# Performance work log

Hardware: AMD Instinct MI355X
Metric: run time of the kernel (lower is better)

## Reference

```python
import jax, jax.numpy as jnp
import numpy as np

NUM_EMBEDDINGS = 4096
EMBEDDING_DIM = 64
COMMITMENT_COST = 0.25


def setup_inputs() -> dict:
    key = jax.random.key(0)
    kz, kw = jax.random.split(key)
    z = jax.random.normal(kz, (16, 4096, EMBEDDING_DIM), dtype=jnp.float32)
    # torch init: uniform_(-1/num_embeddings, 1/num_embeddings)
    W = jax.random.uniform(kw, (NUM_EMBEDDINGS, EMBEDDING_DIM), dtype=jnp.float32,
                           minval=-1.0 / NUM_EMBEDDINGS, maxval=1.0 / NUM_EMBEDDINGS)
    return {"z": z, "W": W}


def reference(z, W):
    d = W.shape[1]
    zf = z.reshape(-1, d)  # [N, d]
    # squared L2 distances via expansion: ||z||^2 + ||w||^2 - 2 z.w -> [N, K]
    distances = (jnp.sum(zf * zf, axis=1, keepdims=True)
                 + jnp.sum(W * W, axis=1)
                 - 2.0 * jnp.matmul(zf, W.T))
    idx = jnp.argmin(distances, axis=1)          # [N]
    z_q = W[idx].reshape(z.shape)                # gather codebook vectors
    loss = jnp.mean(jnp.square(z - jax.lax.stop_gradient(z_q))) * COMMITMENT_COST
    z_q_out = z + jax.lax.stop_gradient(z_q - z)  # straight-through estimator
    return loss, z_q_out
```

## Files before the change

### kernel.cpp

```cpp
#include <hip/hip_runtime.h>
#include <stdint.h>

typedef short short8 __attribute__((ext_vector_type(8)));
typedef float floatx4 __attribute__((ext_vector_type(4)));

#define BIAS 8.0f

__device__ __forceinline__ unsigned short f2bf(float f) {
    unsigned int u = __float_as_uint(f);
    unsigned int r = (u + 0x7FFFu + ((u >> 16) & 1u)) >> 16;
    return (unsigned short)r;
}

__global__ void vq_prep(const float* __restrict__ W, unsigned short* __restrict__ Wsw,
                        float* __restrict__ out0) {
    const int s = blockIdx.x * 256 + threadIdx.x;
    const int T = s >> 7;
    const int h = (s >> 6) & 1;
    const int l = s & 63;
    const int code = T * 16 + (l & 15);
    const float* src = W + code * 64 + h * 32 + (l >> 4) * 8;
    const floatx4* sp = (const floatx4*)src;
    floatx4 f0 = sp[0], f1 = sp[1];
    short8 fr;
    fr[0] = (short)f2bf(-f0[0]); fr[1] = (short)f2bf(-f0[1]);
    fr[2] = (short)f2bf(-f0[2]); fr[3] = (short)f2bf(-f0[3]);
    fr[4] = (short)f2bf(-f1[0]); fr[5] = (short)f2bf(-f1[1]);
    fr[6] = (short)f2bf(-f1[2]); fr[7] = (short)f2bf(-f1[3]);
    ((short8*)Wsw)[s] = fr;
    if (s == 0) *out0 = 0.0f;
}

__launch_bounds__(256)
__attribute__((amdgpu_waves_per_eu(4, 4)))
__global__ void vq_main(const float* __restrict__ z, const float* __restrict__ W,
                        const unsigned short* __restrict__ Wsw, float* __restrict__ out) {
    __shared__ unsigned int pk_lds[256];
    __shared__ float ls[4];

    const int tid  = threadIdx.x;
    const int lane = tid & 63;
    const int cg   = tid >> 6;
    const int l15  = lane & 15;
    const int lq   = lane >> 4;
    const int rowbase = blockIdx.x * 64;

    short8 afrag[4][2];
    #pragma unroll
    for (int mt = 0; mt < 4; ++mt) {
        const float* zp = z + (rowbase + mt * 16 + l15) * 64 + lq * 8;
        #pragma unroll
        for (int h = 0; h < 2; ++h) {
            const floatx4* p = (const floatx4*)(zp + h * 32);
            floatx4 f0 = p[0], f1 = p[1];
            short8 fr;
            fr[0] = (short)f2bf(f0[0]); fr[1] = (short)f2bf(f0[1]);
            fr[2] = (short)f2bf(f0[2]); fr[3] = (short)f2bf(f0[3]);
            fr[4] = (short)f2bf(f1[0]); fr[5] = (short)f2bf(f1[1]);
            fr[6] = (short)f2bf(f1[2]); fr[7] = (short)f2bf(f1[3]);
            afrag[mt][h] = fr;
        }
    }

    const floatx4 bias4 = {BIAS, BIAS, BIAS, BIAS};
    unsigned int minpk[4][4];
    #pragma unroll
    for (int mt = 0; mt < 4; ++mt)
        #pragma unroll
        for (int r = 0; r < 4; ++r) minpk[mt][r] = 0xFFFFFFFFu;

    const short8* __restrict__ bp = (const short8*)Wsw + cg * 8192 + lane;
    unsigned int kidx = (unsigned int)(cg * 1024 + l15);
    #pragma unroll 1
    for (int it = 0; it < 16; ++it) {
        short8 b0 = bp[0 * 64];
        short8 b1 = bp[1 * 64];
        short8 b2 = bp[2 * 64];
        short8 b3 = bp[3 * 64];
        short8 b4 = bp[4 * 64];
        short8 b5 = bp[5 * 64];
        short8 b6 = bp[6 * 64];
        short8 b7 = bp[7 * 64];
        bp += 512;
        #pragma unroll
        for (int sub = 0; sub < 4; ++sub) {
            short8 c0, c1;
            if (sub == 0) { c0 = b0; c1 = b1; }
            else if (sub == 1) { c0 = b2; c1 = b3; }
            else if (sub == 2) { c0 = b4; c1 = b5; }
            else { c0 = b6; c1 = b7; }
            const unsigned int kk = kidx + (unsigned int)(sub * 16);
            #pragma unroll
            for (int mt = 0; mt < 4; ++mt) {
                floatx4 acc = __builtin_amdgcn_mfma_f32_16x16x32_bf16(afrag[mt][0], c0, bias4, 0, 0, 0);
                acc = __builtin_amdgcn_mfma_f32_16x16x32_bf16(afrag[mt][1], c1, acc, 0, 0, 0);
                #pragma unroll
                for (int r = 0; r < 4; ++r) {
                    unsigned int p = __float_as_uint(acc[r]) | kk;
                    minpk[mt][r] = p < minpk[mt][r] ? p : minpk[mt][r];
                }
            }
        }
        kidx += 64;
    }

    #pragma unroll
    for (int mt = 0; mt < 4; ++mt)
        #pragma unroll
        for (int r = 0; r < 4; ++r) {
            unsigned int v = minpk[mt][r];
            #pragma unroll
            for (int m = 1; m < 16; m <<= 1) {
                unsigned int o = (unsigned int)__shfl_xor((int)v, m, 64);
                v = o < v ? o : v;
            }
            if (l15 == 0) pk_lds[cg * 64 + mt * 16 + lq * 4 + r] = v;
        }
    __syncthreads();

    const int rl  = cg * 16 + l15;
    unsigned int v0 = pk_lds[rl];
    unsigned int v1 = pk_lds[64 + rl];
    unsigned int v2 = pk_lds[128 + rl];
    unsigned int v3 = pk_lds[192 + rl];
    unsigned int vm = v0 < v1 ? v0 : v1;
    unsigned int vn = v2 < v3 ? v2 : v3;
    unsigned int idx = (vm < vn ? vm : vn) & 0xFFFu;

    const int row = rowbase + rl;
    float loss = 0.0f;
    #pragma unroll
    for (int h = 0; h < 2; ++h) {
        const floatx4* wp = (const floatx4*)(W + idx * 64 + h * 32 + lq * 8);
        const floatx4* zp = (const floatx4*)(z + row * 64 + h * 32 + lq * 8);
        floatx4* op = (floatx4*)(out + 1 + row * 64 + h * 32 + lq * 8);
        #pragma unroll
        for (int part = 0; part < 2; ++part) {
            floatx4 wv = wp[part];
            floatx4 zv = zp[part];
            op[part] = wv;
            #pragma unroll
            for (int j = 0; j < 4; ++j) {
                float d = zv[j] - wv[j];
                loss = fmaf(d, d, loss);
            }
        }
    }
    #pragma unroll
    for (int m = 1; m < 64; m <<= 1) loss += __shfl_xor(loss, m, 64);
    if (lane == 0) ls[cg] = loss;
    __syncthreads();
    if (tid == 0) {
        float t = (ls[0] + ls[1]) + (ls[2] + ls[3]);
        atomicAdd(out, t * (0.25f / 4194304.0f));
    }
}

extern "C" void kernel_launch(void* const* d_in, const int* in_sizes, int n_in,
                              void* d_out, int out_size, void* d_ws, size_t ws_size,
                              hipStream_t stream) {
    (void)in_sizes; (void)n_in; (void)out_size; (void)ws_size;
    const float* z = (const float*)d_in[0];
    const float* W = (const float*)d_in[1];
    unsigned short* Wsw = (unsigned short*)d_ws;
    float* out = (float*)d_out;

    vq_prep<<<128, 256, 0, stream>>>(W, Wsw, out);
    vq_main<<<1024, 256, 0, stream>>>(z, W, Wsw, out);
}
```

Measured before the change: 114.0 us.

## Split codebook across 8 waves per block and replace atomic loss with partials

Each block now runs 512 threads, with eight waves each scanning 512 codes instead of four waves scanning 1024. This halves the serial MFMA loop per wave and raises occupancy. The epilogue reduces the eight per-wave minima through LDS, then spreads the gather, output and loss work so each thread handles 8 floats. The global atomicAdd is replaced by per-block partial sums and a third single-block reduction kernel, which costs an extra launch and more LDS reduction work.

```diff
diff --git a/kernel.cpp b/kernel.cpp
--- a/kernel.cpp
+++ b/kernel.cpp
@@ -31,12 +31,13 @@
     if (s == 0) *out0 = 0.0f;
 }
 
-__launch_bounds__(256)
-__attribute__((amdgpu_waves_per_eu(4, 4)))
+__launch_bounds__(512, 8)
 __global__ void vq_main(const float* __restrict__ z, const float* __restrict__ W,
-                        const unsigned short* __restrict__ Wsw, float* __restrict__ out) {
-    __shared__ unsigned int pk_lds[256];
-    __shared__ float ls[4];
+                        const unsigned short* __restrict__ Wsw,
+                        float* __restrict__ out, float* __restrict__ partials) {
+    __shared__ unsigned int pk_lds[512];
+    __shared__ unsigned int idx_lds[64];
+    __shared__ float ls[8];
 
     const int tid  = threadIdx.x;
     const int lane = tid & 63;
@@ -69,10 +70,10 @@
         #pragma unroll
         for (int r = 0; r < 4; ++r) minpk[mt][r] = 0xFFFFFFFFu;
 
-    const short8* __restrict__ bp = (const short8*)Wsw + cg * 8192 + lane;
-    unsigned int kidx = (unsigned int)(cg * 1024 + l15);
+    const short8* __restrict__ bp = (const short8*)Wsw + cg * 4096 + lane;
+    unsigned int kidx = (unsigned int)(cg * 512 + l15);
     #pragma unroll 1
-    for (int it = 0; it < 16; ++it) {
+    for (int it = 0; it < 8; ++it) {
         short8 b0 = bp[0 * 64];
         short8 b1 = bp[1 * 64];
         short8 b2 = bp[2 * 64];
@@ -118,42 +119,57 @@
         }
     __syncthreads();
 
-    const int rl  = cg * 16 + l15;
-    unsigned int v0 = pk_lds[rl];
-    unsigned int v1 = pk_lds[64 + rl];
-    unsigned int v2 = pk_lds[128 + rl];
-    unsigned int v3 = pk_lds[192 + rl];
-    unsigned int vm = v0 < v1 ? v0 : v1;
-    unsigned int vn = v2 < v3 ? v2 : v3;
-    unsigned int idx = (vm < vn ? vm : vn) & 0xFFFu;
+    if (tid < 64) {
+        unsigned int v = pk_lds[tid];
+        #pragma unroll
+        for (int j = 1; j < 8; ++j) {
+            unsigned int u = pk_lds[j * 64 + tid];
+            v = u < v ? u : v;
+        }
+        idx_lds[tid] = v & 0xFFFu;
+    }
+    __syncthreads();
 
-    const int row = rowbase + rl;
+    const int rloc = tid >> 3;
+    const int seg  = (tid & 7) * 8;
+    const unsigned int idx = idx_lds[rloc];
+    const int row = rowbase + rloc;
+    const floatx4* wp = (const floatx4*)(W + idx * 64 + seg);
+    const floatx4* zp = (const floatx4*)(z + row * 64 + seg);
+    floatx4* op = (floatx4*)(out + 1 + row * 64 + seg);
+    floatx4 w0 = wp[0], w1 = wp[1];
+    floatx4 z0 = zp[0], z1 = zp[1];
+    op[0] = w0; op[1] = w1;
     float loss = 0.0f;
     #pragma unroll
-    for (int h = 0; h < 2; ++h) {
-        const floatx4* wp = (const floatx4*)(W + idx * 64 + h * 32 + lq * 8);
-        const floatx4* zp = (const floatx4*)(z + row * 64 + h * 32 + lq * 8);
-        floatx4* op = (floatx4*)(out + 1 + row * 64 + h * 32 + lq * 8);
-        #pragma unroll
-        for (int part = 0; part < 2; ++part) {
-            floatx4 wv = wp[part];
-            floatx4 zv = zp[part];
-            op[part] = wv;
-            #pragma unroll
-            for (int j = 0; j < 4; ++j) {
-                float d = zv[j] - wv[j];
-                loss = fmaf(d, d, loss);
-            }
-        }
+    for (int j = 0; j < 4; ++j) {
+        float d0 = z0[j] - w0[j];
+        float d1 = z1[j] - w1[j];
+        loss = fmaf(d0, d0, loss);
+        loss = fmaf(d1, d1, loss);
     }
     #pragma unroll
     for (int m = 1; m < 64; m <<= 1) loss += __shfl_xor(loss, m, 64);
     if (lane == 0) ls[cg] = loss;
     __syncthreads();
     if (tid == 0) {
-        float t = (ls[0] + ls[1]) + (ls[2] + ls[3]);
-        atomicAdd(out, t * (0.25f / 4194304.0f));
+        float t = ((ls[0] + ls[1]) + (ls[2] + ls[3]))
+                + ((ls[4] + ls[5]) + (ls[6] + ls[7]));
+        partials[blockIdx.x] = t;
     }
+}
+
+__global__ void vq_loss(const float* __restrict__ partials, float* __restrict__ out) {
+    __shared__ float ls[4];
+    const int tid  = threadIdx.x;
+    const int lane = tid & 63;
+    const int w    = tid >> 6;
+    float s = partials[tid] + partials[tid + 256] + partials[tid + 512] + partials[tid + 768];
+    #pragma unroll
+    for (int m = 1; m < 64; m <<= 1) s += __shfl_xor(s, m, 64);
+    if (lane == 0) ls[w] = s;
+    __syncthreads();
+    if (tid == 0) out[0] = ((ls[0] + ls[1]) + (ls[2] + ls[3])) * (0.25f / 4194304.0f);
 }
 
 extern "C" void kernel_launch(void* const* d_in, const int* in_sizes, int n_in,
@@ -163,8 +179,10 @@
     const float* z = (const float*)d_in[0];
     const float* W = (const float*)d_in[1];
     unsigned short* Wsw = (unsigned short*)d_ws;
+    float* partials = (float*)((char*)d_ws + (512 << 10));
     float* out = (float*)d_out;
 
     vq_prep<<<128, 256, 0, stream>>>(W, Wsw, out);
-    vq_main<<<1024, 256, 0, stream>>>(z, W, Wsw, out);
+    vq_main<<<1024, 512, 0, stream>>>(z, W, Wsw, out, partials);
+    vq_loss<<<1, 256, 0, stream>>>(partials, out);
 }
```

New measurement: 447.7 us. +292.7%, slower.
